# Kernel optimization log

Hardware: AMD Instinct MI355X
Metric: run time of the kernel (lower is better)

## Reference

```python
import jax, jax.numpy as jnp
import numpy as np
from jax import lax

V, E, H = 32000, 512, 512
B, S = 64, 512

def setup_inputs() -> dict:
    key = jax.random.key(0)
    k1, k2, k3, k4, k5 = jax.random.split(key, 5)
    bound = 1.0 / np.sqrt(H)  # torch nn.RNN init: U(-1/sqrt(H), 1/sqrt(H))
    return {
        "input_tensor": jax.random.randint(k1, (B, S), 0, V, dtype=jnp.int64),
        "emb": jax.random.normal(k2, (V, E), dtype=jnp.float32),  # nn.Embedding ~ N(0,1)
        "W_ih": jax.random.uniform(k3, (H, E), jnp.float32, -bound, bound),
        "W_hh": jax.random.uniform(k4, (H, H), jnp.float32, -bound, bound),
        "b_ih": jax.random.uniform(k5, (H,), jnp.float32, -bound, bound),
        "b_hh": jax.random.uniform(jax.random.fold_in(key, 7), (H,), jnp.float32, -bound, bound),
    }

def reference(input_tensor, emb, W_ih, W_hh, b_ih, b_hh):
    # Embedding lookup: (B, S, E)
    x = emb[input_tensor]
    # Precompute input projection for all timesteps (batched GEMM): (B, S, H)
    x_proj = jnp.einsum("bse,he->bsh", x, W_ih) + b_ih + b_hh
    h0 = jnp.zeros((B, H), dtype=x.dtype)

    def step(h, xp_t):  # xp_t: (B, H)
        h_new = jnp.tanh(xp_t + h @ W_hh.T)
        return h_new, h_new

    hT, outs = lax.scan(step, h0, jnp.swapaxes(x_proj, 0, 1))  # outs: (S, B, H)
    outputs = jnp.swapaxes(outs, 0, 1)  # (B, S, H), batch_first
    hidden = hT[None]  # (1, B, H) matching torch (num_layers, B, H)
    return outputs, hidden
```

## Files before the change

### kernel.cpp

```cpp
#include <hip/hip_runtime.h>
#include <cstdint>

#define BB 64
#define SS 512
#define HH 512
#define EE 512
#define BSH (BB*SS*HH)

typedef _Float16 f16x8 __attribute__((ext_vector_type(8)));
typedef float    f32x4 __attribute__((ext_vector_type(4)));
typedef int      iv4   __attribute__((ext_vector_type(4)));
typedef unsigned long long u64;

__device__ __forceinline__ f16x8 pack8(float4 u, float4 v) {
    f16x8 h;
    h[0] = (_Float16)u.x; h[1] = (_Float16)u.y;
    h[2] = (_Float16)u.z; h[3] = (_Float16)u.w;
    h[4] = (_Float16)v.x; h[5] = (_Float16)v.y;
    h[6] = (_Float16)v.z; h[7] = (_Float16)v.w;
    return h;
}

#define SW (127.0f * 22.627416997969522f)

__device__ __forceinline__ int quanw(float x) {
    return (int)rintf(fminf(fmaxf(x * SW, -127.0f), 127.0f));
}
__device__ __forceinline__ int packw4(float4 f) {
    int q0 = quanw(f.x), q1 = quanw(f.y), q2 = quanw(f.z), q3 = quanw(f.w);
    return (q0 & 255) | ((q1 & 255) << 8) | ((q2 & 255) << 16) | (q3 << 24);
}

__device__ __forceinline__ void gload16(const void* g, void* l) {
    __builtin_amdgcn_global_load_lds(
        (const __attribute__((address_space(1))) void*)g,
        (__attribute__((address_space(3))) void*)l, 16, 0, 0);
}

__global__ __launch_bounds__(256) void prep(
    const int* __restrict__ idx, const float* __restrict__ emb,
    const float* __restrict__ Wih, _Float16* __restrict__ a16,
    _Float16* __restrict__ b16) {
    const int bid = blockIdx.x, tid = threadIdx.x;
    if (bid < 8192) {
        int e = bid * 2048 + tid * 8;
        int m = e >> 9, c = e & 511;
        int gi = idx[m];
        const float* s = emb + (size_t)gi * EE + c;
        float4 u = *(const float4*)s, v = *(const float4*)(s + 4);
        *(f16x8*)(a16 + e) = pack8(u, v);
    } else {
        int e = (bid - 8192) * 2048 + tid * 8;
        float4 u = *(const float4*)(Wih + e), v = *(const float4*)(Wih + e + 4);
        *(f16x8*)(b16 + e) = pack8(u, v);
    }
}

__global__ __launch_bounds__(256, 3) void phase1h(
    const _Float16* __restrict__ a16, const _Float16* __restrict__ b16,
    const float* __restrict__ bih, const float* __restrict__ bhh,
    float* __restrict__ out) {
    __shared__ __align__(16) _Float16 Al[128 * 64];
    __shared__ __align__(16) _Float16 Bl[128 * 64];

    const int tid  = threadIdx.x;
    const int xcd  = blockIdx.x & 7;
    const int slot = blockIdx.x >> 3;
    const int m0   = ((slot >> 2) * 8 + xcd) * 128;
    const int n0   = (slot & 3) * 128;
    const int wv   = tid >> 6;
    const int lane = tid & 63;
    const int n    = lane & 15;
    const int quad = lane >> 4;
    const int mw   = wv >> 1;
    const int nw   = wv & 1;

    const int srow = wv * 8 + (lane >> 3);
    const int scol = (lane & 7) * 8;
    const _Float16* agl = a16 + (size_t)(m0 + srow) * EE + scol;
    const _Float16* bgl = b16 + (size_t)(n0 + srow) * EE + scol;
    _Float16* al = Al + wv * 512;
    _Float16* bl = Bl + wv * 512;

    f32x4 acc[4][4];
#pragma unroll
    for (int a = 0; a < 4; ++a)
#pragma unroll
        for (int c = 0; c < 4; ++c) acc[a][c] = (f32x4){0.f, 0.f, 0.f, 0.f};

    for (int kc = 0; kc < 8; ++kc) {
#pragma unroll
        for (int i = 0; i < 4; ++i)
            gload16(agl + (size_t)i * 32 * EE + kc * 64, al + i * 2048);
#pragma unroll
        for (int i = 0; i < 4; ++i)
            gload16(bgl + (size_t)i * 32 * EE + kc * 64, bl + i * 2048);
        __syncthreads();

#pragma unroll
        for (int kk = 0; kk < 2; ++kk) {
            f16x8 bfr[4];
#pragma unroll
            for (int nb = 0; nb < 4; ++nb)
                bfr[nb] = *(const f16x8*)&Bl[(nw * 64 + nb * 16 + n) * 64 + kk * 32 + quad * 8];
#pragma unroll
            for (int mb = 0; mb < 4; ++mb) {
                f16x8 afr = *(const f16x8*)&Al[(mw * 64 + mb * 16 + n) * 64 + kk * 32 + quad * 8];
#pragma unroll
                for (int nb = 0; nb < 4; ++nb)
                    acc[mb][nb] = __builtin_amdgcn_mfma_f32_16x16x32_f16(
                        afr, bfr[nb], acc[mb][nb], 0, 0, 0);
            }
        }
        __syncthreads();
    }

    int   cc[4];
    float bv[4];
#pragma unroll
    for (int nb = 0; nb < 4; ++nb) {
        cc[nb] = n0 + nw * 64 + nb * 16 + n;
        bv[nb] = bih[cc[nb]] + bhh[cc[nb]];
    }
#pragma unroll
    for (int mb = 0; mb < 4; ++mb) {
        int rowg = m0 + mw * 64 + mb * 16 + quad * 4;
#pragma unroll
        for (int nb = 0; nb < 4; ++nb) {
#pragma unroll
            for (int i = 0; i < 4; ++i)
                out[(size_t)(rowg + i) * HH + cc[nb]] = acc[mb][nb][i] + bv[nb];
        }
    }
}

__global__ __launch_bounds__(256, 3) void phase1(
    const int* __restrict__ idx, const float* __restrict__ emb,
    const float* __restrict__ Wih, const float* __restrict__ bih,
    const float* __restrict__ bhh, float* __restrict__ out) {
    __shared__ __align__(16) _Float16 Al[128 * 72];
    __shared__ __align__(16) _Float16 Bl[128 * 72];

    const int tid  = threadIdx.x;
    const int xcd  = blockIdx.x & 7;
    const int slot = blockIdx.x >> 3;
    const int m0   = ((slot >> 2) * 8 + xcd) * 128;
    const int n0   = (slot & 3) * 128;
    const int wv   = tid >> 6;
    const int lane = tid & 63;
    const int n    = lane & 15;
    const int quad = lane >> 4;
    const int mw   = wv >> 1;
    const int nw   = wv & 1;

    const int sr = tid >> 1;
    const int kh = (tid & 1) * 32;
    const int rowidx = idx[m0 + sr];
    const float* ap = emb + (size_t)rowidx * EE + kh;
    const float* bp = Wih + (size_t)(n0 + sr) * EE + kh;

    f32x4 acc[4][4];
#pragma unroll
    for (int a = 0; a < 4; ++a)
#pragma unroll
        for (int c = 0; c < 4; ++c) acc[a][c] = (f32x4){0.f, 0.f, 0.f, 0.f};

    for (int kc = 0; kc < 8; ++kc) {
#pragma unroll
        for (int q = 0; q < 4; ++q) {
            float4 u = *(const float4*)(ap + kc * 64 + q * 8);
            float4 v = *(const float4*)(ap + kc * 64 + q * 8 + 4);
            *(f16x8*)&Al[sr * 72 + kh + q * 8] = pack8(u, v);
        }
#pragma unroll
        for (int q = 0; q < 4; ++q) {
            float4 u = *(const float4*)(bp + kc * 64 + q * 8);
            float4 v = *(const float4*)(bp + kc * 64 + q * 8 + 4);
            *(f16x8*)&Bl[sr * 72 + kh + q * 8] = pack8(u, v);
        }
        __syncthreads();

#pragma unroll
        for (int kk = 0; kk < 2; ++kk) {
            f16x8 bfr[4];
#pragma unroll
            for (int nb = 0; nb < 4; ++nb)
                bfr[nb] = *(const f16x8*)&Bl[(nw * 64 + nb * 16 + n) * 72 + kk * 32 + quad * 8];
#pragma unroll
            for (int mb = 0; mb < 4; ++mb) {
                f16x8 afr = *(const f16x8*)&Al[(mw * 64 + mb * 16 + n) * 72 + kk * 32 + quad * 8];
#pragma unroll
                for (int nb = 0; nb < 4; ++nb)
                    acc[mb][nb] = __builtin_amdgcn_mfma_f32_16x16x32_f16(
                        afr, bfr[nb], acc[mb][nb], 0, 0, 0);
            }
        }
        __syncthreads();
    }

    int   cc[4];
    float bv[4];
#pragma unroll
    for (int nb = 0; nb < 4; ++nb) {
        cc[nb] = n0 + nw * 64 + nb * 16 + n;
        bv[nb] = bih[cc[nb]] + bhh[cc[nb]];
    }
#pragma unroll
    for (int mb = 0; mb < 4; ++mb) {
        int rowg = m0 + mw * 64 + mb * 16 + quad * 4;
#pragma unroll
        for (int nb = 0; nb < 4; ++nb) {
#pragma unroll
            for (int i = 0; i < 4; ++i)
                out[(size_t)(rowg + i) * HH + cc[nb]] = acc[mb][nb][i] + bv[nb];
        }
    }
}

__global__ __launch_bounds__(512, 1) void phase2(
    const float* __restrict__ Whh, float* __restrict__ out) {
    __shared__ __align__(16) unsigned char himg[2][512];

    const int tid  = threadIdx.x;
    const int b    = blockIdx.x;
    const int wv   = tid >> 6;
    const int lane = tid & 63;
    const int n    = lane & 15;
    const int quad = lane >> 4;

    iv4 areg[4][8];
#pragma unroll
    for (int mb = 0; mb < 4; ++mb) {
        const float* wr = Whh + (size_t)(wv * 64 + mb * 16 + n) * HH + quad * 16;
#pragma unroll
        for (int j = 0; j < 8; ++j) {
            int kb = (j < 7) ? ((wv + 1 + j) & 7) : wv;
            const float4* p = (const float4*)(wr + kb * 64);
            iv4 v;
            v[0] = packw4(p[0]);
            v[1] = packw4(p[1]);
            v[2] = packw4(p[2]);
            v[3] = packw4(p[3]);
            areg[mb][j] = v;
        }
    }
    if (tid < 64) ((u64*)himg[0])[tid] = 0ull;
    __syncthreads();

    const int  ilo = n & 1;
    const int  ihi = (n >> 1) & 1;
    const bool sb0 = ((n >> 2) & 1) != 0;
    const bool sb1 = ((n >> 3) & 1) != 0;
    const int  row = wv * 64 + ((n >> 2) & 3) * 16 + quad * 4 + (n & 3);
    float* obase = out + (size_t)b * (SS * HH) + row;

    int koff[7];
#pragma unroll
    for (int j = 0; j < 7; ++j) koff[j] = ((wv + 1 + j) & 7) * 64 + quad * 16;
    const int oown = wv * 64 + quad * 16;

    const float inv2 = (2.0f * 1.4426950408889634f) / (SW * 127.0f);
    const float K2   = 2.0f * 1.4426950408889634f;

    iv4 acc0 = (iv4){0,0,0,0}, acc1 = (iv4){0,0,0,0};
    iv4 acc2 = (iv4){0,0,0,0}, acc3 = (iv4){0,0,0,0};

    float xp2_c = obase[0] * K2;
    float xp2_n = obase[HH] * K2;
    float hl = 0.f;
    unsigned char* h0p = himg[0];
    unsigned char* h1p = himg[1];

#define RNN_STEP(T, HBR, HNX)                                                  \
    {                                                                          \
         \
        float xp_f = obase[(size_t)((T) + 2) * HH];                            \
        _Pragma("unroll")                                                      \
        for (int j = 0; j < 7; ++j) {                                          \
            iv4 bfr = *(const iv4*)((HBR) + koff[j]);                          \
            acc0 = __builtin_amdgcn_mfma_i32_16x16x64_i8(areg[0][j], bfr, acc0, 0, 0, 0); \
            acc1 = __builtin_amdgcn_mfma_i32_16x16x64_i8(areg[1][j], bfr, acc1, 0, 0, 0); \
            acc2 = __builtin_amdgcn_mfma_i32_16x16x64_i8(areg[2][j], bfr, acc2, 0, 0, 0); \
            acc3 = __builtin_amdgcn_mfma_i32_16x16x64_i8(areg[3][j], bfr, acc3, 0, 0, 0); \
        }                                                                      \
        iv4 sa = sb0 ? acc1 : acc0;                                            \
        iv4 sc = sb0 ? acc3 : acc2;                                            \
        iv4 s  = sb1 ? sc : sa;                                                \
        int zA = ilo ? s[1] : s[0];                                            \
        int zB = ilo ? s[3] : s[2];                                            \
        int z  = ihi ? zB : zA;                                                \
        float u  = fmaf((float)z, inv2, xp2_c);                                \
        float ex;                                                              \
        __asm__("v_exp_f32 %0, %1" : "=v"(ex) : "v"(u));                       \
        float r  = __builtin_amdgcn_rcpf(ex + 1.0f);                           \
        int   q  = (int)rintf(fmaf(r, -254.0f, 127.0f));                       \
        *(char*)((HNX) + row) = (char)q;                                       \
        iv4 bown = *(const iv4*)((HNX) + oown);                                \
        acc0 = __builtin_amdgcn_mfma_i32_16x16x64_i8(areg[0][7], bown, (iv4){0,0,0,0}, 0, 0, 0); \
        acc1 = __builtin_amdgcn_mfma_i32_16x16x64_i8(areg[1][7], bown, (iv4){0,0,0,0}, 0, 0, 0); \
        acc2 = __builtin_amdgcn_mfma_i32_16x16x64_i8(areg[2][7], bown, (iv4){0,0,0,0}, 0, 0, 0); \
        acc3 = __builtin_amdgcn_mfma_i32_16x16x64_i8(areg[3][7], bown, (iv4){0,0,0,0}, 0, 0, 0); \
        float h = fmaf(r, -2.0f, 1.0f);                                        \
        obase[(size_t)(T) * HH] = h;                                           \
        hl = h;                                                                \
        __builtin_amdgcn_sched_barrier(0);                                     \
        __asm__ volatile("s_waitcnt lgkmcnt(0)\n\ts_barrier" ::: "memory");    \
        xp2_c = xp2_n; xp2_n = xp_f * K2;                                      \
    }

    for (int t = 0; t < SS; t += 2) {
        RNN_STEP(t,     h0p, h1p);
        RNN_STEP(t + 1, h1p, h0p);
    }
#undef RNN_STEP

    out[BSH + (size_t)b * HH + row] = hl;
}

extern "C" void kernel_launch(void* const* d_in, const int* in_sizes, int n_in,
                              void* d_out, int out_size, void* d_ws, size_t ws_size,
                              hipStream_t stream) {
    const int*   idx = (const int*)d_in[0];
    const float* emb = (const float*)d_in[1];
    const float* Wih = (const float*)d_in[2];
    const float* Whh = (const float*)d_in[3];
    const float* bih = (const float*)d_in[4];
    const float* bhh = (const float*)d_in[5];
    float* out = (float*)d_out;

    const size_t needA = (size_t)BB * SS * EE * sizeof(_Float16);
    const size_t needB = (size_t)HH * EE * sizeof(_Float16);

    if (d_ws && ws_size >= needA + needB) {
        _Float16* a16 = (_Float16*)d_ws;
        _Float16* b16 = (_Float16*)((char*)d_ws + needA);
        prep<<<dim3(8192 + 128), dim3(256), 0, stream>>>(idx, emb, Wih, a16, b16);
        phase1h<<<dim3(1024), dim3(256), 0, stream>>>(a16, b16, bih, bhh, out);
    } else {
        phase1<<<dim3(1024), dim3(256), 0, stream>>>(idx, emb, Wih, bih, bhh, out);
    }
    phase2<<<dim3(64), dim3(512), 0, stream>>>(Whh, out);
}
```

Before: 547.2 us.

## Fuse input projection GEMM and recurrence into one persistent kernel with tile counters

Merges the projection GEMM and the recurrent scan into a single launch. The first 64 blocks run the recurrence, and the remaining 1024 blocks compute projection tiles ordered by time chunk. Each GEMM block bumps a per-chunk atomic counter when its tile is written, and recurrence blocks spin on that counter before entering each 128-step chunk. The aim is to overlap the GEMM with the sequential recurrence and drop a kernel boundary. The cost is spin-wait overhead, a smaller 128x128 tile split across 8 waves, and reliance on the GEMM blocks getting scheduled while the recurrence blocks occupy CUs.

```diff
diff --git a/kernel.cpp b/kernel.cpp
--- a/kernel.cpp
+++ b/kernel.cpp
@@ -35,6 +35,13 @@
     __builtin_amdgcn_global_load_lds(
         (const __attribute__((address_space(1))) void*)g,
         (__attribute__((address_space(3))) void*)l, 16, 0, 0);
+}
+
+__device__ __forceinline__ void wait_tile(const unsigned int* c, unsigned int tgt) {
+    while (__hip_atomic_load(c, __ATOMIC_RELAXED, __HIP_MEMORY_SCOPE_AGENT) < tgt) {
+        __builtin_amdgcn_s_sleep(2);
+    }
+    __builtin_amdgcn_fence(__ATOMIC_ACQUIRE, "agent");
 }
 
 __global__ __launch_bounds__(256) void prep(
@@ -56,177 +63,102 @@
     }
 }
 
-__global__ __launch_bounds__(256, 3) void phase1h(
+__global__ __launch_bounds__(512, 1) void fused12(
     const _Float16* __restrict__ a16, const _Float16* __restrict__ b16,
     const float* __restrict__ bih, const float* __restrict__ bhh,
-    float* __restrict__ out) {
-    __shared__ __align__(16) _Float16 Al[128 * 64];
-    __shared__ __align__(16) _Float16 Bl[128 * 64];
+    const float* __restrict__ Whh, float* __restrict__ out,
+    unsigned int* __restrict__ cnt) {
+    __shared__ __align__(16) unsigned char smem[32768];
 
     const int tid  = threadIdx.x;
-    const int xcd  = blockIdx.x & 7;
-    const int slot = blockIdx.x >> 3;
-    const int m0   = ((slot >> 2) * 8 + xcd) * 128;
-    const int n0   = (slot & 3) * 128;
+    const int bid  = blockIdx.x;
     const int wv   = tid >> 6;
     const int lane = tid & 63;
     const int n    = lane & 15;
     const int quad = lane >> 4;
-    const int mw   = wv >> 1;
-    const int nw   = wv & 1;
-
-    const int srow = wv * 8 + (lane >> 3);
-    const int scol = (lane & 7) * 8;
-    const _Float16* agl = a16 + (size_t)(m0 + srow) * EE + scol;
-    const _Float16* bgl = b16 + (size_t)(n0 + srow) * EE + scol;
-    _Float16* al = Al + wv * 512;
-    _Float16* bl = Bl + wv * 512;
-
-    f32x4 acc[4][4];
-#pragma unroll
-    for (int a = 0; a < 4; ++a)
-#pragma unroll
-        for (int c = 0; c < 4; ++c) acc[a][c] = (f32x4){0.f, 0.f, 0.f, 0.f};
-
-    for (int kc = 0; kc < 8; ++kc) {
-#pragma unroll
-        for (int i = 0; i < 4; ++i)
-            gload16(agl + (size_t)i * 32 * EE + kc * 64, al + i * 2048);
-#pragma unroll
-        for (int i = 0; i < 4; ++i)
-            gload16(bgl + (size_t)i * 32 * EE + kc * 64, bl + i * 2048);
+
+    if (bid >= 64) {
+        _Float16* Al = (_Float16*)smem;
+        _Float16* Bl = (_Float16*)(smem + 16384);
+        const int p  = bid - 64;
+        const int st = p >> 8;
+        const int r  = p & 255;
+        const int bb = r >> 2;
+        const int nt = r & 3;
+        const int m0 = bb * 512 + st * 128;
+        const int n0 = nt * 128;
+
+        const int srow = wv * 16 + (lane >> 3);
+        const int scol = (lane & 7) * 8;
+        const _Float16* agl = a16 + (size_t)(m0 + srow) * EE + scol;
+        const _Float16* bgl = b16 + (size_t)(n0 + srow) * EE + scol;
+        _Float16* al = Al + wv * 1024;
+        _Float16* bl = Bl + wv * 1024;
+
+        const int mw = wv >> 2;
+        const int nw = wv & 3;
+
+        f32x4 acc[4][2];
+#pragma unroll
+        for (int mb = 0; mb < 4; ++mb)
+#pragma unroll
+            for (int nb = 0; nb < 2; ++nb) acc[mb][nb] = (f32x4){0.f, 0.f, 0.f, 0.f};
+
+        for (int kc = 0; kc < 8; ++kc) {
+            gload16(agl + kc * 64,               al);
+            gload16(agl + (size_t)8 * EE + kc * 64, al + 512);
+            gload16(bgl + kc * 64,               bl);
+            gload16(bgl + (size_t)8 * EE + kc * 64, bl + 512);
+            __syncthreads();
+
+#pragma unroll
+            for (int kk = 0; kk < 2; ++kk) {
+                f16x8 bfr[2];
+#pragma unroll
+                for (int nb = 0; nb < 2; ++nb)
+                    bfr[nb] = *(const f16x8*)&Bl[(nw * 32 + nb * 16 + n) * 64 + kk * 32 + quad * 8];
+#pragma unroll
+                for (int mb = 0; mb < 4; ++mb) {
+                    f16x8 afr = *(const f16x8*)&Al[(mw * 64 + mb * 16 + n) * 64 + kk * 32 + quad * 8];
+#pragma unroll
+                    for (int nb = 0; nb < 2; ++nb)
+                        acc[mb][nb] = __builtin_amdgcn_mfma_f32_16x16x32_f16(
+                            afr, bfr[nb], acc[mb][nb], 0, 0, 0);
+                }
+            }
+            __syncthreads();
+        }
+
+        int   cc[2];
+        float bv[2];
+#pragma unroll
+        for (int nb = 0; nb < 2; ++nb) {
+            cc[nb] = n0 + nw * 32 + nb * 16 + n;
+            bv[nb] = bih[cc[nb]] + bhh[cc[nb]];
+        }
+#pragma unroll
+        for (int mb = 0; mb < 4; ++mb) {
+            int rowg = m0 + mw * 64 + mb * 16 + quad * 4;
+#pragma unroll
+            for (int nb = 0; nb < 2; ++nb) {
+#pragma unroll
+                for (int i = 0; i < 4; ++i)
+                    out[(size_t)(rowg + i) * HH + cc[nb]] = acc[mb][nb][i] + bv[nb];
+            }
+        }
+        __asm__ volatile("s_waitcnt vmcnt(0)" ::: "memory");
         __syncthreads();
-
-#pragma unroll
-        for (int kk = 0; kk < 2; ++kk) {
-            f16x8 bfr[4];
-#pragma unroll
-            for (int nb = 0; nb < 4; ++nb)
-                bfr[nb] = *(const f16x8*)&Bl[(nw * 64 + nb * 16 + n) * 64 + kk * 32 + quad * 8];
-#pragma unroll
-            for (int mb = 0; mb < 4; ++mb) {
-                f16x8 afr = *(const f16x8*)&Al[(mw * 64 + mb * 16 + n) * 64 + kk * 32 + quad * 8];
-#pragma unroll
-                for (int nb = 0; nb < 4; ++nb)
-                    acc[mb][nb] = __builtin_amdgcn_mfma_f32_16x16x32_f16(
-                        afr, bfr[nb], acc[mb][nb], 0, 0, 0);
-            }
-        }
-        __syncthreads();
-    }
-
-    int   cc[4];
-    float bv[4];
-#pragma unroll
-    for (int nb = 0; nb < 4; ++nb) {
-        cc[nb] = n0 + nw * 64 + nb * 16 + n;
-        bv[nb] = bih[cc[nb]] + bhh[cc[nb]];
-    }
-#pragma unroll
-    for (int mb = 0; mb < 4; ++mb) {
-        int rowg = m0 + mw * 64 + mb * 16 + quad * 4;
-#pragma unroll
-        for (int nb = 0; nb < 4; ++nb) {
-#pragma unroll
-            for (int i = 0; i < 4; ++i)
-                out[(size_t)(rowg + i) * HH + cc[nb]] = acc[mb][nb][i] + bv[nb];
-        }
-    }
-}
-
-__global__ __launch_bounds__(256, 3) void phase1(
-    const int* __restrict__ idx, const float* __restrict__ emb,
-    const float* __restrict__ Wih, const float* __restrict__ bih,
-    const float* __restrict__ bhh, float* __restrict__ out) {
-    __shared__ __align__(16) _Float16 Al[128 * 72];
-    __shared__ __align__(16) _Float16 Bl[128 * 72];
-
-    const int tid  = threadIdx.x;
-    const int xcd  = blockIdx.x & 7;
-    const int slot = blockIdx.x >> 3;
-    const int m0   = ((slot >> 2) * 8 + xcd) * 128;
-    const int n0   = (slot & 3) * 128;
-    const int wv   = tid >> 6;
-    const int lane = tid & 63;
-    const int n    = lane & 15;
-    const int quad = lane >> 4;
-    const int mw   = wv >> 1;
-    const int nw   = wv & 1;
-
-    const int sr = tid >> 1;
-    const int kh = (tid & 1) * 32;
-    const int rowidx = idx[m0 + sr];
-    const float* ap = emb + (size_t)rowidx * EE + kh;
-    const float* bp = Wih + (size_t)(n0 + sr) * EE + kh;
-
-    f32x4 acc[4][4];
-#pragma unroll
-    for (int a = 0; a < 4; ++a)
-#pragma unroll
-        for (int c = 0; c < 4; ++c) acc[a][c] = (f32x4){0.f, 0.f, 0.f, 0.f};
-
-    for (int kc = 0; kc < 8; ++kc) {
-#pragma unroll
-        for (int q = 0; q < 4; ++q) {
-            float4 u = *(const float4*)(ap + kc * 64 + q * 8);
-            float4 v = *(const float4*)(ap + kc * 64 + q * 8 + 4);
-            *(f16x8*)&Al[sr * 72 + kh + q * 8] = pack8(u, v);
-        }
-#pragma unroll
-        for (int q = 0; q < 4; ++q) {
-            float4 u = *(const float4*)(bp + kc * 64 + q * 8);
-            float4 v = *(const float4*)(bp + kc * 64 + q * 8 + 4);
-            *(f16x8*)&Bl[sr * 72 + kh + q * 8] = pack8(u, v);
-        }
-        __syncthreads();
-
-#pragma unroll
-        for (int kk = 0; kk < 2; ++kk) {
-            f16x8 bfr[4];
-#pragma unroll
-            for (int nb = 0; nb < 4; ++nb)
-                bfr[nb] = *(const f16x8*)&Bl[(nw * 64 + nb * 16 + n) * 72 + kk * 32 + quad * 8];
-#pragma unroll
-            for (int mb = 0; mb < 4; ++mb) {
-                f16x8 afr = *(const f16x8*)&Al[(mw * 64 + mb * 16 + n) * 72 + kk * 32 + quad * 8];
-#pragma unroll
-                for (int nb = 0; nb < 4; ++nb)
-                    acc[mb][nb] = __builtin_amdgcn_mfma_f32_16x16x32_f16(
-                        afr, bfr[nb], acc[mb][nb], 0, 0, 0);
-            }
-        }
-        __syncthreads();
-    }
-
-    int   cc[4];
-    float bv[4];
-#pragma unroll
-    for (int nb = 0; nb < 4; ++nb) {
-        cc[nb] = n0 + nw * 64 + nb * 16 + n;
-        bv[nb] = bih[cc[nb]] + bhh[cc[nb]];
-    }
-#pragma unroll
-    for (int mb = 0; mb < 4; ++mb) {
-        int rowg = m0 + mw * 64 + mb * 16 + quad * 4;
-#pragma unroll
-        for (int nb = 0; nb < 4; ++nb) {
-#pragma unroll
-            for (int i = 0; i < 4; ++i)
-                out[(size_t)(rowg + i) * HH + cc[nb]] = acc[mb][nb][i] + bv[nb];
-        }
-    }
-}
-
-__global__ __launch_bounds__(512, 1) void phase2(
-    const float* __restrict__ Whh, float* __restrict__ out) {
-    __shared__ __align__(16) unsigned char himg[2][512];
-
-    const int tid  = threadIdx.x;
-    const int b    = blockIdx.x;
-    const int wv   = tid >> 6;
-    const int lane = tid & 63;
-    const int n    = lane & 15;
-    const int quad = lane >> 4;
+        if (tid == 0) {
+            __builtin_amdgcn_fence(__ATOMIC_RELEASE, "agent");
+            __hip_atomic_fetch_add(cnt + st, 1u, __ATOMIC_RELAXED,
+                                   __HIP_MEMORY_SCOPE_AGENT);
+        }
+        return;
+    }
+
+    unsigned char* h0p = smem;
+    unsigned char* h1p = smem + 512;
+    const int b = bid;
 
     iv4 areg[4][8];
 #pragma unroll
@@ -235,16 +167,16 @@
 #pragma unroll
         for (int j = 0; j < 8; ++j) {
             int kb = (j < 7) ? ((wv + 1 + j) & 7) : wv;
-            const float4* p = (const float4*)(wr + kb * 64);
+            const float4* ptr = (const float4*)(wr + kb * 64);
             iv4 v;
-            v[0] = packw4(p[0]);
-            v[1] = packw4(p[1]);
-            v[2] = packw4(p[2]);
-            v[3] = packw4(p[3]);
+            v[0] = packw4(ptr[0]);
+            v[1] = packw4(ptr[1]);
+            v[2] = packw4(ptr[2]);
+            v[3] = packw4(ptr[3]);
             areg[mb][j] = v;
         }
     }
-    if (tid < 64) ((u64*)himg[0])[tid] = 0ull;
+    if (tid < 64) ((u64*)h0p)[tid] = 0ull;
     __syncthreads();
 
     const int  ilo = n & 1;
@@ -265,15 +197,15 @@
     iv4 acc0 = (iv4){0,0,0,0}, acc1 = (iv4){0,0,0,0};
     iv4 acc2 = (iv4){0,0,0,0}, acc3 = (iv4){0,0,0,0};
 
+    wait_tile(cnt, 256u);
     float xp2_c = obase[0] * K2;
     float xp2_n = obase[HH] * K2;
     float hl = 0.f;
-    unsigned char* h0p = himg[0];
-    unsigned char* h1p = himg[1];
 
 #define RNN_STEP(T, HBR, HNX)                                                  \
     {                                                                          \
-         \
+        if ((((T) + 2) & 127) == 0 && ((T) + 2) < SS)                          \
+            wait_tile(cnt + (((T) + 2) >> 7), 256u);                           \
         float xp_f = obase[(size_t)((T) + 2) * HH];                            \
         _Pragma("unroll")                                                      \
         for (int j = 0; j < 7; ++j) {                                          \
@@ -292,15 +224,195 @@
         float u  = fmaf((float)z, inv2, xp2_c);                                \
         float ex;                                                              \
         __asm__("v_exp_f32 %0, %1" : "=v"(ex) : "v"(u));                       \
-        float r  = __builtin_amdgcn_rcpf(ex + 1.0f);                           \
-        int   q  = (int)rintf(fmaf(r, -254.0f, 127.0f));                       \
+        float rr = __builtin_amdgcn_rcpf(ex + 1.0f);                           \
+        int   q  = (int)rintf(fmaf(rr, -254.0f, 127.0f));                      \
         *(char*)((HNX) + row) = (char)q;                                       \
         iv4 bown = *(const iv4*)((HNX) + oown);                                \
         acc0 = __builtin_amdgcn_mfma_i32_16x16x64_i8(areg[0][7], bown, (iv4){0,0,0,0}, 0, 0, 0); \
         acc1 = __builtin_amdgcn_mfma_i32_16x16x64_i8(areg[1][7], bown, (iv4){0,0,0,0}, 0, 0, 0); \
         acc2 = __builtin_amdgcn_mfma_i32_16x16x64_i8(areg[2][7], bown, (iv4){0,0,0,0}, 0, 0, 0); \
         acc3 = __builtin_amdgcn_mfma_i32_16x16x64_i8(areg[3][7], bown, (iv4){0,0,0,0}, 0, 0, 0); \
-        float h = fmaf(r, -2.0f, 1.0f);                                        \
+        float h = fmaf(rr, -2.0f, 1.0f);                                       \
+        obase[(size_t)(T) * HH] = h;                                           \
+        hl = h;                                                                \
+        __builtin_amdgcn_sched_barrier(0);                                     \
+        __asm__ volatile("s_waitcnt lgkmcnt(0)\n\ts_barrier" ::: "memory");    \
+        xp2_c = xp2_n; xp2_n = xp_f * K2;                                      \
+    }
+
+    for (int t = 0; t < SS; t += 2) {
+        RNN_STEP(t,     h0p, h1p);
+        RNN_STEP(t + 1, h1p, h0p);
+    }
+#undef RNN_STEP
+
+    out[BSH + (size_t)b * HH + row] = hl;
+}
+
+__global__ __launch_bounds__(256, 3) void phase1(
+    const int* __restrict__ idx, const float* __restrict__ emb,
+    const float* __restrict__ Wih, const float* __restrict__ bih,
+    const float* __restrict__ bhh, float* __restrict__ out) {
+    __shared__ __align__(16) _Float16 Al[128 * 72];
+    __shared__ __align__(16) _Float16 Bl[128 * 72];
+
+    const int tid  = threadIdx.x;
+    const int m0   = (blockIdx.x >> 2) * 128;
+    const int n0   = (blockIdx.x & 3) * 128;
+    const int wv   = tid >> 6;
+    const int lane = tid & 63;
+    const int n    = lane & 15;
+    const int quad = lane >> 4;
+    const int mw   = wv >> 1;
+    const int nw   = wv & 1;
+
+    const int sr = tid >> 1;
+    const int kh = (tid & 1) * 32;
+    const int rowidx = idx[m0 + sr];
+    const float* ap = emb + (size_t)rowidx * EE + kh;
+    const float* bp = Wih + (size_t)(n0 + sr) * EE + kh;
+
+    f32x4 acc[4][4];
+#pragma unroll
+    for (int a = 0; a < 4; ++a)
+#pragma unroll
+        for (int c = 0; c < 4; ++c) acc[a][c] = (f32x4){0.f, 0.f, 0.f, 0.f};
+
+    for (int kc = 0; kc < 8; ++kc) {
+#pragma unroll
+        for (int q = 0; q < 4; ++q) {
+            float4 u = *(const float4*)(ap + kc * 64 + q * 8);
+            float4 v = *(const float4*)(ap + kc * 64 + q * 8 + 4);
+            *(f16x8*)&Al[sr * 72 + kh + q * 8] = pack8(u, v);
+        }
+#pragma unroll
+        for (int q = 0; q < 4; ++q) {
+            float4 u = *(const float4*)(bp + kc * 64 + q * 8);
+            float4 v = *(const float4*)(bp + kc * 64 + q * 8 + 4);
+            *(f16x8*)&Bl[sr * 72 + kh + q * 8] = pack8(u, v);
+        }
+        __syncthreads();
+
+#pragma unroll
+        for (int kk = 0; kk < 2; ++kk) {
+            f16x8 bfr[4];
+#pragma unroll
+            for (int nb = 0; nb < 4; ++nb)
+                bfr[nb] = *(const f16x8*)&Bl[(nw * 64 + nb * 16 + n) * 72 + kk * 32 + quad * 8];
+#pragma unroll
+            for (int mb = 0; mb < 4; ++mb) {
+                f16x8 afr = *(const f16x8*)&Al[(mw * 64 + mb * 16 + n) * 72 + kk * 32 + quad * 8];
+#pragma unroll
+                for (int nb = 0; nb < 4; ++nb)
+                    acc[mb][nb] = __builtin_amdgcn_mfma_f32_16x16x32_f16(
+                        afr, bfr[nb], acc[mb][nb], 0, 0, 0);
+            }
+        }
+        __syncthreads();
+    }
+
+    int   cc[4];
+    float bv[4];
+#pragma unroll
+    for (int nb = 0; nb < 4; ++nb) {
+        cc[nb] = n0 + nw * 64 + nb * 16 + n;
+        bv[nb] = bih[cc[nb]] + bhh[cc[nb]];
+    }
+#pragma unroll
+    for (int mb = 0; mb < 4; ++mb) {
+        int rowg = m0 + mw * 64 + mb * 16 + quad * 4;
+#pragma unroll
+        for (int nb = 0; nb < 4; ++nb) {
+#pragma unroll
+            for (int i = 0; i < 4; ++i)
+                out[(size_t)(rowg + i) * HH + cc[nb]] = acc[mb][nb][i] + bv[nb];
+        }
+    }
+}
+
+__global__ __launch_bounds__(512, 1) void phase2(
+    const float* __restrict__ Whh, float* __restrict__ out) {
+    __shared__ __align__(16) unsigned char himg[2][512];
+
+    const int tid  = threadIdx.x;
+    const int b    = blockIdx.x;
+    const int wv   = tid >> 6;
+    const int lane = tid & 63;
+    const int n    = lane & 15;
+    const int quad = lane >> 4;
+
+    iv4 areg[4][8];
+#pragma unroll
+    for (int mb = 0; mb < 4; ++mb) {
+        const float* wr = Whh + (size_t)(wv * 64 + mb * 16 + n) * HH + quad * 16;
+#pragma unroll
+        for (int j = 0; j < 8; ++j) {
+            int kb = (j < 7) ? ((wv + 1 + j) & 7) : wv;
+            const float4* p = (const float4*)(wr + kb * 64);
+            iv4 v;
+            v[0] = packw4(p[0]);
+            v[1] = packw4(p[1]);
+            v[2] = packw4(p[2]);
+            v[3] = packw4(p[3]);
+            areg[mb][j] = v;
+        }
+    }
+    if (tid < 64) ((u64*)himg[0])[tid] = 0ull;
+    __syncthreads();
+
+    const int  ilo = n & 1;
+    const int  ihi = (n >> 1) & 1;
+    const bool sb0 = ((n >> 2) & 1) != 0;
+    const bool sb1 = ((n >> 3) & 1) != 0;
+    const int  row = wv * 64 + ((n >> 2) & 3) * 16 + quad * 4 + (n & 3);
+    float* obase = out + (size_t)b * (SS * HH) + row;
+
+    int koff[7];
+#pragma unroll
+    for (int j = 0; j < 7; ++j) koff[j] = ((wv + 1 + j) & 7) * 64 + quad * 16;
+    const int oown = wv * 64 + quad * 16;
+
+    const float inv2 = (2.0f * 1.4426950408889634f) / (SW * 127.0f);
+    const float K2   = 2.0f * 1.4426950408889634f;
+
+    iv4 acc0 = (iv4){0,0,0,0}, acc1 = (iv4){0,0,0,0};
+    iv4 acc2 = (iv4){0,0,0,0}, acc3 = (iv4){0,0,0,0};
+
+    float xp2_c = obase[0] * K2;
+    float xp2_n = obase[HH] * K2;
+    float hl = 0.f;
+    unsigned char* h0p = himg[0];
+    unsigned char* h1p = himg[1];
+
+#define RNN_STEP(T, HBR, HNX)                                                  \
+    {                                                                          \
+        float xp_f = obase[(size_t)((T) + 2) * HH];                            \
+        _Pragma("unroll")                                                      \
+        for (int j = 0; j < 7; ++j) {                                          \
+            iv4 bfr = *(const iv4*)((HBR) + koff[j]);                          \
+            acc0 = __builtin_amdgcn_mfma_i32_16x16x64_i8(areg[0][j], bfr, acc0, 0, 0, 0); \
+            acc1 = __builtin_amdgcn_mfma_i32_16x16x64_i8(areg[1][j], bfr, acc1, 0, 0, 0); \
+            acc2 = __builtin_amdgcn_mfma_i32_16x16x64_i8(areg[2][j], bfr, acc2, 0, 0, 0); \
+            acc3 = __builtin_amdgcn_mfma_i32_16x16x64_i8(areg[3][j], bfr, acc3, 0, 0, 0); \
+        }                                                                      \
+        iv4 sa = sb0 ? acc1 : acc0;                                            \
+        iv4 sc = sb0 ? acc3 : acc2;                                            \
+        iv4 s  = sb1 ? sc : sa;                                                \
+        int zA = ilo ? s[1] : s[0];                                            \
+        int zB = ilo ? s[3] : s[2];                                            \
+        int z  = ihi ? zB : zA;                                                \
+        float u  = fmaf((float)z, inv2, xp2_c);                                \
+        float ex;                                                              \
+        __asm__("v_exp_f32 %0, %1" : "=v"(ex) : "v"(u));                       \
+        float rr = __builtin_amdgcn_rcpf(ex + 1.0f);                           \
+        int   q  = (int)rintf(fmaf(rr, -254.0f, 127.0f));                      \
+        *(char*)((HNX) + row) = (char)q;                                       \
+        iv4 bown = *(const iv4*)((HNX) + oown);                                \
+        acc0 = __builtin_amdgcn_mfma_i32_16x16x64_i8(areg[0][7], bown, (iv4){0,0,0,0}, 0, 0, 0); \
+        acc1 = __builtin_amdgcn_mfma_i32_16x16x64_i8(areg[1][7], bown, (iv4){0,0,0,0}, 0, 0, 0); \
+        acc2 = __builtin_amdgcn_mfma_i32_16x16x64_i8(areg[2][7], bown, (iv4){0,0,0,0}, 0, 0, 0); \
+        acc3 = __builtin_amdgcn_mfma_i32_16x16x64_i8(areg[3][7], bown, (iv4){0,0,0,0}, 0, 0, 0); \
+        float h = fmaf(rr, -2.0f, 1.0f);                                       \
         obase[(size_t)(T) * HH] = h;                                           \
         hl = h;                                                                \
         __builtin_amdgcn_sched_barrier(0);                                     \
@@ -330,14 +442,19 @@
 
     const size_t needA = (size_t)BB * SS * EE * sizeof(_Float16);
     const size_t needB = (size_t)HH * EE * sizeof(_Float16);
-
-    if (d_ws && ws_size >= needA + needB) {
+    const size_t CNTOFF = needA + needB;
+    const size_t needT = CNTOFF + 4 * sizeof(unsigned int);
+
+    if (d_ws && ws_size >= needT) {
         _Float16* a16 = (_Float16*)d_ws;
         _Float16* b16 = (_Float16*)((char*)d_ws + needA);
+        unsigned int* cnt = (unsigned int*)((char*)d_ws + CNTOFF);
+        hipMemsetAsync(cnt, 0, 4 * sizeof(unsigned int), stream);
         prep<<<dim3(8192 + 128), dim3(256), 0, stream>>>(idx, emb, Wih, a16, b16);
-        phase1h<<<dim3(1024), dim3(256), 0, stream>>>(a16, b16, bih, bhh, out);
+        fused12<<<dim3(64 + 1024), dim3(512), 0, stream>>>(
+            a16, b16, bih, bhh, Whh, out, cnt);
     } else {
         phase1<<<dim3(1024), dim3(256), 0, stream>>>(idx, emb, Wih, bih, bhh, out);
-    }
-    phase2<<<dim3(64), dim3(512), 0, stream>>>(Whh, out);
-}
+        phase2<<<dim3(64), dim3(512), 0, stream>>>(Whh, out);
+    }
+}
```

Result: no change. 553.0 us (+1.1%).
